# Performance work log

Hardware: AMD Instinct MI355X
Metric: run time of the kernel (lower is better)

The kernel has to match this reference:

```python
import jax, jax.numpy as jnp
import numpy as np

N_ATOMS = 200_000
AVG_NEIGHBORS = 64
N_PAIRS = N_ATOMS * AVG_NEIGHBORS
BOX = 60.0  # Angstrom, so cutoff=10 masks most random pairs (realistic neighbor-list sparsity)


def setup_inputs() -> dict:
    key = jax.random.key(0)
    kR, ki, kj = jax.random.split(key, 3)
    R = jax.random.uniform(kR, (N_ATOMS, 3), dtype=jnp.float32) * BOX
    idx_i = jax.random.randint(ki, (N_PAIRS,), 0, N_ATOMS, dtype=jnp.int32)
    idx_j = jax.random.randint(kj, (N_PAIRS,), 0, N_ATOMS, dtype=jnp.int32)
    # learned scalar parameters from __init__
    epsilon = jnp.float32(0.238)
    sigma = jnp.float32(3.4)
    cutoff = jnp.float32(10.0)
    return {"R": R, "epsilon": epsilon, "sigma": sigma, "cutoff": cutoff,
            "idx_i": idx_i, "idx_j": idx_j}


def reference(R, epsilon, sigma, cutoff, idx_i, idx_j):
    """LJ 12-6 pairwise potential over a neighbor list.

    Returns (energy [N] per-atom, forces [N,3]).
    Each (i,j) pair appears in both directions in the pair list, hence the 0.5
    factor on per-atom energy; forces accumulate per direction (action-reaction
    handled by the symmetric pair list).
    """
    n_atoms = R.shape[0]
    rij = R[idx_i] - R[idx_j]                     # [P,3] gather
    r2 = jnp.sum(rij * rij, axis=-1)              # [P]
    mask = (r2 < cutoff * cutoff) & (r2 > 1e-10)  # inside cutoff, exclude coincident
    r2s = jnp.where(mask, r2, 1.0)                # safe divide
    sr2 = (sigma * sigma) / r2s
    sr6 = sr2 * sr2 * sr2
    sr12 = sr6 * sr6
    e_pair = jnp.where(mask, 4.0 * epsilon * (sr12 - sr6), 0.0)          # [P]
    f_mag = jnp.where(mask, 24.0 * epsilon * (2.0 * sr12 - sr6) / r2s, 0.0)
    f_pair = f_mag[:, None] * rij                 # [P,3]
    energy = 0.5 * jax.ops.segment_sum(e_pair, idx_i, num_segments=n_atoms)   # [N]
    forces = jax.ops.segment_sum(f_pair, idx_i, num_segments=n_atoms)         # [N,3]
    return energy, forces
```

## Files before the change

kernel.cpp:

```cpp
#include <hip/hip_runtime.h>
#include <stdint.h>


typedef int   v4i __attribute__((ext_vector_type(4)));
typedef float v4f __attribute__((ext_vector_type(4)));
typedef float v2f __attribute__((ext_vector_type(2)));

#define GRP    8
#define WGT    1024
#define NWG_F  256

#if __has_builtin(__builtin_amdgcn_global_atomic_fadd_v2f32)
__device__ __forceinline__ void pk_atomic_add(float* p, float a, float b) {
    typedef __attribute__((address_space(1))) v2f gv2f;
    v2f v; v.x = a; v.y = b;
    (void)__builtin_amdgcn_global_atomic_fadd_v2f32((gv2f*)(uintptr_t)p, v);
}
#else
__device__ __forceinline__ void pk_atomic_add(float* p, float a, float b) {
    atomicAdd(p, a);
    atomicAdd(p + 1, b);
}
#endif

__global__ void __launch_bounds__(256) prep_kernel(
    const float* __restrict__ R, const float* __restrict__ cut_p,
    v4f* __restrict__ Rp, unsigned* __restrict__ packed, int n_atoms)
{
    int t = blockIdx.x * blockDim.x + threadIdx.x;
    int n_grp = (n_atoms + 4) / 5;
    if (t >= n_grp) return;
    const float inv_cut = 1.0f / cut_p[0];
    int a0 = t * 5;
    unsigned w = 0u;
#pragma unroll
    for (int k = 0; k < 5; ++k) {
        int a = a0 + k;
        if (a < n_atoms) {
            float x = R[3 * a + 0];
            float y = R[3 * a + 1];
            float z = R[3 * a + 2];
            v4f v; v.x = x; v.y = y; v.z = z; v.w = 0.0f;
            Rp[a] = v;
            int cx = min(7, max(0, (int)(x * inv_cut)));
            int cy = min(7, max(0, (int)(y * inv_cut)));
            w |= (unsigned)(cx | (cy << 3)) << (6 * k);
        }
    }
    packed[t] = w;
}

__global__ void __launch_bounds__(256) pad_R_kernel(
    const float* __restrict__ R, v4f* __restrict__ Rp, int n_atoms)
{
    int a = blockIdx.x * blockDim.x + threadIdx.x;
    if (a < n_atoms) {
        v4f v;
        v.x = R[3 * a + 0];
        v.y = R[3 * a + 1];
        v.z = R[3 * a + 2];
        v.w = 0.0f;
        Rp[a] = v;
    }
}

__device__ __forceinline__ unsigned cell6w(const unsigned* __restrict__ lds32,
                                           unsigned a) {
    unsigned q = __umulhi(a, 0xCCCCCCCDu) >> 2;
    unsigned r = a - q * 5u;
    return (lds32[q] >> (r * 6u)) & 63u;
}

__device__ __forceinline__ void load_grp(
    const int* __restrict__ idx_i, const int* __restrict__ idx_j,
    int p, int n_pairs, int* __restrict__ is8, int* __restrict__ js8)
{
    if (p + GRP <= n_pairs) {
        v4i a0 = __builtin_nontemporal_load((const v4i*)idx_i + (p >> 2));
        v4i a1 = __builtin_nontemporal_load((const v4i*)idx_i + (p >> 2) + 1);
        v4i b0 = __builtin_nontemporal_load((const v4i*)idx_j + (p >> 2));
        v4i b1 = __builtin_nontemporal_load((const v4i*)idx_j + (p >> 2) + 1);
        is8[0] = a0.x; is8[1] = a0.y; is8[2] = a0.z; is8[3] = a0.w;
        is8[4] = a1.x; is8[5] = a1.y; is8[6] = a1.z; is8[7] = a1.w;
        js8[0] = b0.x; js8[1] = b0.y; js8[2] = b0.z; js8[3] = b0.w;
        js8[4] = b1.x; js8[5] = b1.y; js8[6] = b1.z; js8[7] = b1.w;
    } else {
#pragma unroll
        for (int k = 0; k < GRP; ++k) {
            bool v = (p + k < n_pairs);
            is8[k] = v ? idx_i[p + k] : 0;
            js8[k] = v ? idx_j[p + k] : 0;
        }
    }
}

__device__ __forceinline__ void filt_sel(const unsigned* __restrict__ lds32,
                                         int* __restrict__ is8,
                                         int* __restrict__ js8)
{
#pragma unroll
    for (int k = 0; k < GRP; ++k) {
        unsigned ci = cell6w(lds32, (unsigned)is8[k]);
        unsigned cj = cell6w(lds32, (unsigned)js8[k]);
        int ddx = (int)(ci & 7u) - (int)(cj & 7u);
        int ddy = (int)(ci >> 3) - (int)(cj >> 3);
        bool ok = ((unsigned)(ddx + 1) <= 2u) & ((unsigned)(ddy + 1) <= 2u);
        is8[k] = ok ? is8[k] : 0;
        js8[k] = ok ? js8[k] : 0;
    }
}

__device__ __forceinline__ void lj_body_st(
    v4f A, v4f B, float eps, float s2, float cut2, int gi,
    float* __restrict__ st)
{
    const float dx = A.x - B.x, dy = A.y - B.y, dz = A.z - B.z;
    const float r2 = dx * dx + dy * dy + dz * dz;
    if (r2 < cut2 && r2 > 1e-10f) {
        const float inv  = 1.0f / r2;
        const float sr2  = s2 * inv;
        const float sr6  = sr2 * sr2 * sr2;
        const float sr12 = sr6 * sr6;
        const float e    = 2.0f * eps * (sr12 - sr6);
        const float f    = 24.0f * eps * (2.0f * sr12 - sr6) * inv;
        float* p = st + ((size_t)(unsigned)gi << 2);
        pk_atomic_add(p,     e,      f * dx);
        pk_atomic_add(p + 2, f * dy, f * dz);
    }
}

__device__ __forceinline__ void lj_body(
    v4f A, v4f B, float eps, float s2, float cut2, int gi,
    float* __restrict__ energy, float* __restrict__ forces)
{
    const float dx = A.x - B.x, dy = A.y - B.y, dz = A.z - B.z;
    const float r2 = dx * dx + dy * dy + dz * dz;
    if (r2 < cut2 && r2 > 1e-10f) {
        const float inv  = 1.0f / r2;
        const float sr2  = s2 * inv;
        const float sr6  = sr2 * sr2 * sr2;
        const float sr12 = sr6 * sr6;
        const float e    = 2.0f * eps * (sr12 - sr6);
        const float f    = 24.0f * eps * (2.0f * sr12 - sr6) * inv;
        atomicAdd(&energy[gi], e);
        atomicAdd(&forces[3 * gi + 0], f * dx);
        atomicAdd(&forces[3 * gi + 1], f * dy);
        atomicAdd(&forces[3 * gi + 2], f * dz);
    }
}

__global__ void __launch_bounds__(WGT, 4) lj_fused_st_kernel(
    const v4f* __restrict__ Rp,
    const unsigned* __restrict__ packed,
    const int* __restrict__ idx_i,
    const int* __restrict__ idx_j,
    const float* __restrict__ eps_p,
    const float* __restrict__ sig_p,
    const float* __restrict__ cut_p,
    float* __restrict__ st,
    int n_pairs, int pk_words, int chunk)
{
    extern __shared__ unsigned lds[];
    for (int w = threadIdx.x; w < pk_words; w += WGT)
        lds[w] = packed[w];
    __syncthreads();

    const float eps  = eps_p[0];
    const float sig  = sig_p[0];
    const float cut  = cut_p[0];
    const float s2   = sig * sig;
    const float cut2 = cut * cut;

    const int cs = blockIdx.x * chunk;
    const int ce = min(cs + chunk, n_pairs);
    const int STRIDE = WGT * GRP;

    int p0 = cs + (int)threadIdx.x * GRP;
    if (p0 >= ce) return;

    int isA[GRP], jsA[GRP], isB[GRP], jsB[GRP];

    load_grp(idx_i, idx_j, p0, n_pairs, isA, jsA);
    filt_sel(lds, isA, jsA);
    int p1 = p0 + STRIDE;

    while (true) {
        const bool h1 = p1 < ce;

        if (h1) load_grp(idx_i, idx_j, p1, n_pairs, isB, jsB);

        v4f Ri[GRP], Rj[GRP];
#pragma unroll
        for (int k = 0; k < GRP; ++k) { Ri[k] = Rp[isA[k]]; Rj[k] = Rp[jsA[k]]; }

        if (h1) filt_sel(lds, isB, jsB);

#pragma unroll
        for (int k = 0; k < GRP; ++k)
            lj_body_st(Ri[k], Rj[k], eps, s2, cut2, isA[k], st);

        if (!h1) break;
#pragma unroll
        for (int k = 0; k < GRP; ++k) { isA[k] = isB[k]; jsA[k] = jsB[k]; }
        p1 += STRIDE;
    }
}

__global__ void __launch_bounds__(256) finalize_kernel(
    const v4f* __restrict__ st, float* __restrict__ energy,
    float* __restrict__ forces, int n_atoms)
{
    int a = blockIdx.x * blockDim.x + threadIdx.x;
    if (a < n_atoms) {
        v4f s = st[a];
        energy[a]          = s.x;
        forces[3 * a + 0]  = s.y;
        forces[3 * a + 1]  = s.z;
        forces[3 * a + 2]  = s.w;
    }
}

__global__ void __launch_bounds__(WGT, 4) lj_fused_kernel(
    const v4f* __restrict__ Rp,
    const unsigned* __restrict__ packed,
    const int* __restrict__ idx_i,
    const int* __restrict__ idx_j,
    const float* __restrict__ eps_p,
    const float* __restrict__ sig_p,
    const float* __restrict__ cut_p,
    float* __restrict__ energy,
    float* __restrict__ forces,
    int n_pairs, int pk_words, int chunk)
{
    extern __shared__ unsigned lds[];
    for (int w = threadIdx.x; w < pk_words; w += WGT)
        lds[w] = packed[w];
    __syncthreads();

    const float eps  = eps_p[0];
    const float sig  = sig_p[0];
    const float cut  = cut_p[0];
    const float s2   = sig * sig;
    const float cut2 = cut * cut;

    const int cs = blockIdx.x * chunk;
    const int ce = min(cs + chunk, n_pairs);
    const int STRIDE = WGT * GRP;

    int p0 = cs + (int)threadIdx.x * GRP;
    if (p0 >= ce) return;

    int isA[GRP], jsA[GRP], isB[GRP], jsB[GRP];
    load_grp(idx_i, idx_j, p0, n_pairs, isA, jsA);
    filt_sel(lds, isA, jsA);
    int p1 = p0 + STRIDE;

    while (true) {
        const bool h1 = p1 < ce;
        if (h1) load_grp(idx_i, idx_j, p1, n_pairs, isB, jsB);
        v4f Ri[GRP], Rj[GRP];
#pragma unroll
        for (int k = 0; k < GRP; ++k) { Ri[k] = Rp[isA[k]]; Rj[k] = Rp[jsA[k]]; }
        if (h1) filt_sel(lds, isB, jsB);
#pragma unroll
        for (int k = 0; k < GRP; ++k)
            lj_body(Ri[k], Rj[k], eps, s2, cut2, isA[k], energy, forces);
        if (!h1) break;
#pragma unroll
        for (int k = 0; k < GRP; ++k) { isA[k] = isB[k]; jsA[k] = jsB[k]; }
        p1 += STRIDE;
    }
}

#define PPT 8
__global__ void __launch_bounds__(256) lj_pairs_fb_kernel(
    const v4f* __restrict__ Rp,
    const v4i* __restrict__ idx_i4, const v4i* __restrict__ idx_j4,
    const float* __restrict__ eps_p, const float* __restrict__ sig_p,
    const float* __restrict__ cut_p,
    float* __restrict__ energy, float* __restrict__ forces, int n_oct)
{
    int t = blockIdx.x * blockDim.x + threadIdx.x;
    if (t >= n_oct) return;
    const float eps  = eps_p[0];
    const float sig  = sig_p[0];
    const float cut  = cut_p[0];
    const float s2   = sig * sig;
    const float cut2 = cut * cut;
    v4i ii0 = __builtin_nontemporal_load(idx_i4 + 2 * t);
    v4i ii1 = __builtin_nontemporal_load(idx_i4 + 2 * t + 1);
    v4i jj0 = __builtin_nontemporal_load(idx_j4 + 2 * t);
    v4i jj1 = __builtin_nontemporal_load(idx_j4 + 2 * t + 1);
    int is[PPT] = { ii0.x, ii0.y, ii0.z, ii0.w, ii1.x, ii1.y, ii1.z, ii1.w };
    int js[PPT] = { jj0.x, jj0.y, jj0.z, jj0.w, jj1.x, jj1.y, jj1.z, jj1.w };
    v4f Ri[PPT], Rj[PPT];
#pragma unroll
    for (int k = 0; k < PPT; ++k) Ri[k] = Rp[is[k]];
#pragma unroll
    for (int k = 0; k < PPT; ++k) Rj[k] = Rp[js[k]];
#pragma unroll
    for (int k = 0; k < PPT; ++k)
        lj_body(Ri[k], Rj[k], eps, s2, cut2, is[k], energy, forces);
}

__global__ void lj_pairs_fb_tail_kernel(
    const v4f* __restrict__ Rp,
    const int* __restrict__ idx_i, const int* __restrict__ idx_j,
    const float* __restrict__ eps_p, const float* __restrict__ sig_p,
    const float* __restrict__ cut_p,
    float* __restrict__ energy, float* __restrict__ forces,
    int start, int n_pairs)
{
    int p = start + blockIdx.x * blockDim.x + threadIdx.x;
    if (p >= n_pairs) return;
    const float eps = eps_p[0];
    const float sig = sig_p[0];
    const float cut = cut_p[0];
    lj_body(Rp[idx_i[p]], Rp[idx_j[p]], eps, sig * sig, cut * cut,
            idx_i[p], energy, forces);
}

extern "C" void kernel_launch(void* const* d_in, const int* in_sizes, int n_in,
                              void* d_out, int out_size, void* d_ws, size_t ws_size,
                              hipStream_t stream) {
    const float* R     = (const float*)d_in[0];
    const float* eps_p = (const float*)d_in[1];
    const float* sig_p = (const float*)d_in[2];
    const float* cut_p = (const float*)d_in[3];
    const int*   idx_i = (const int*)d_in[4];
    const int*   idx_j = (const int*)d_in[5];

    const int n_atoms = in_sizes[0] / 3;
    const int n_pairs = in_sizes[4];

    float* energy = (float*)d_out;
    float* forces = (float*)d_out + n_atoms;

    char* ws = (char*)d_ws;
    const size_t rp_b     = (((size_t)n_atoms * 16) + 255) & ~(size_t)255;
    const int    pk_words = (n_atoms + 4) / 5;
    const size_t pk_b     = (((size_t)pk_words * 4) + 255) & ~(size_t)255;
    const size_t st_b     = (((size_t)n_atoms * 16) + 255) & ~(size_t)255;
    const size_t lds_b    = (((size_t)pk_words * 4) + 15) & ~(size_t)15;

    const bool have_rp  = ws_size >= rp_b;
    const bool lds_ok   = lds_b <= 160000;
    const bool use_st   = have_rp && lds_ok
                          && (ws_size >= rp_b + pk_b + st_b);
    const bool use_old  = !use_st && have_rp && lds_ok
                          && (ws_size >= rp_b + pk_b);

    v4f*      Rp     = (v4f*)ws;
    unsigned* packed = (unsigned*)(ws + rp_b);
    float*    st     = (float*)(ws + rp_b + pk_b);

    if (use_st) {
        (void)hipMemsetAsync(st, 0, (size_t)n_atoms * 16, stream);

        int pblocks = (pk_words + 255) / 256;
        prep_kernel<<<pblocks, 256, 0, stream>>>(R, cut_p, Rp, packed, n_atoms);

        (void)hipFuncSetAttribute((const void*)lj_fused_st_kernel,
                                  hipFuncAttributeMaxDynamicSharedMemorySize,
                                  (int)lds_b);
        int chunk = (((n_pairs + NWG_F - 1) / NWG_F) + GRP - 1) & ~(GRP - 1);
        lj_fused_st_kernel<<<NWG_F, WGT, lds_b, stream>>>(
            Rp, packed, idx_i, idx_j, eps_p, sig_p, cut_p,
            st, n_pairs, pk_words, chunk);

        int fblocks = (n_atoms + 255) / 256;
        finalize_kernel<<<fblocks, 256, 0, stream>>>(
            (const v4f*)st, energy, forces, n_atoms);
    } else if (use_old) {
        (void)hipMemsetAsync(d_out, 0, (size_t)out_size * sizeof(float), stream);

        int pblocks = (pk_words + 255) / 256;
        prep_kernel<<<pblocks, 256, 0, stream>>>(R, cut_p, Rp, packed, n_atoms);

        (void)hipFuncSetAttribute((const void*)lj_fused_kernel,
                                  hipFuncAttributeMaxDynamicSharedMemorySize,
                                  (int)lds_b);
        int chunk = (((n_pairs + NWG_F - 1) / NWG_F) + GRP - 1) & ~(GRP - 1);
        lj_fused_kernel<<<NWG_F, WGT, lds_b, stream>>>(
            Rp, packed, idx_i, idx_j, eps_p, sig_p, cut_p,
            energy, forces, n_pairs, pk_words, chunk);
    } else if (have_rp) {
        (void)hipMemsetAsync(d_out, 0, (size_t)out_size * sizeof(float), stream);

        int blocks = (n_atoms + 255) / 256;
        pad_R_kernel<<<blocks, 256, 0, stream>>>(R, Rp, n_atoms);
        const int n_oct = n_pairs / PPT;
        const int start = n_oct * PPT;
        if (n_oct > 0) {
            int fblocks = (n_oct + 255) / 256;
            lj_pairs_fb_kernel<<<fblocks, 256, 0, stream>>>(
                Rp, (const v4i*)idx_i, (const v4i*)idx_j,
                eps_p, sig_p, cut_p, energy, forces, n_oct);
        }
        if (start < n_pairs) {
            lj_pairs_fb_tail_kernel<<<1, 64, 0, stream>>>(
                Rp, idx_i, idx_j, eps_p, sig_p, cut_p,
                energy, forces, start, n_pairs);
        }
    }
}
```

Baseline: 191.0 us.

## Compact passing pairs per wave via ballot and LDS before issuing atomics

The 6-bit cell codes are now packed densely, 16 atoms per 3 words, and read as unaligned byte pairs from LDS, which frees LDS space. In that space each wave gets a small staging buffer. Passing LJ pairs are compacted into it with ballot/mbcnt, and the lanes then issue atomics from the packed buffer, so atomics run on contiguous active lanes instead of sparse divergent ones. In exchange, the packed v2f atomics are replaced by four scalar atomics, LDS traffic and wave-uniform loop control are added, and pairs that overflow the buffer fall back to direct atomics.

```diff
diff --git a/kernel.cpp b/kernel.cpp
--- a/kernel.cpp
+++ b/kernel.cpp
@@ -4,38 +4,27 @@
 
 typedef int   v4i __attribute__((ext_vector_type(4)));
 typedef float v4f __attribute__((ext_vector_type(4)));
-typedef float v2f __attribute__((ext_vector_type(2)));
 
 #define GRP    8
 #define WGT    1024
 #define NWG_F  256
-
-#if __has_builtin(__builtin_amdgcn_global_atomic_fadd_v2f32)
-__device__ __forceinline__ void pk_atomic_add(float* p, float a, float b) {
-    typedef __attribute__((address_space(1))) v2f gv2f;
-    v2f v; v.x = a; v.y = b;
-    (void)__builtin_amdgcn_global_atomic_fadd_v2f32((gv2f*)(uintptr_t)p, v);
-}
-#else
-__device__ __forceinline__ void pk_atomic_add(float* p, float a, float b) {
-    atomicAdd(p, a);
-    atomicAdd(p + 1, b);
-}
-#endif
+#define SLOTS  31
 
 __global__ void __launch_bounds__(256) prep_kernel(
     const float* __restrict__ R, const float* __restrict__ cut_p,
     v4f* __restrict__ Rp, unsigned* __restrict__ packed, int n_atoms)
 {
     int t = blockIdx.x * blockDim.x + threadIdx.x;
-    int n_grp = (n_atoms + 4) / 5;
-    if (t >= n_grp) return;
+    int n_thr = (n_atoms + 15) >> 4;
+    if (t == 0) packed[3 * n_thr] = 0u;
+    if (t >= n_thr) return;
     const float inv_cut = 1.0f / cut_p[0];
-    int a0 = t * 5;
-    unsigned w = 0u;
-#pragma unroll
-    for (int k = 0; k < 5; ++k) {
+    int a0 = t << 4;
+    unsigned w[3] = {0u, 0u, 0u};
+#pragma unroll
+    for (int k = 0; k < 16; ++k) {
         int a = a0 + k;
+        unsigned c = 0u;
         if (a < n_atoms) {
             float x = R[3 * a + 0];
             float y = R[3 * a + 1];
@@ -44,10 +33,15 @@
             Rp[a] = v;
             int cx = min(7, max(0, (int)(x * inv_cut)));
             int cy = min(7, max(0, (int)(y * inv_cut)));
-            w |= (unsigned)(cx | (cy << 3)) << (6 * k);
-        }
-    }
-    packed[t] = w;
+            c = (unsigned)(cx | (cy << 3));
+        }
+        int bit = 6 * k, word = bit >> 5, off = bit & 31;
+        w[word] |= c << off;
+        if (off > 26) w[word + 1] |= c >> (32 - off);
+    }
+    packed[3 * t + 0] = w[0];
+    packed[3 * t + 1] = w[1];
+    packed[3 * t + 2] = w[2];
 }
 
 __global__ void __launch_bounds__(256) pad_R_kernel(
@@ -64,11 +58,11 @@
     }
 }
 
-__device__ __forceinline__ unsigned cell6w(const unsigned* __restrict__ lds32,
-                                           unsigned a) {
-    unsigned q = __umulhi(a, 0xCCCCCCCDu) >> 2;
-    unsigned r = a - q * 5u;
-    return (lds32[q] >> (r * 6u)) & 63u;
+__device__ __forceinline__ unsigned cell6(const unsigned char* c8, unsigned a) {
+    unsigned bit = a * 6u;
+    unsigned by  = bit >> 3;
+    unsigned v   = (unsigned)c8[by] | ((unsigned)c8[by + 1] << 8);
+    return (v >> (bit & 7u)) & 63u;
 }
 
 __device__ __forceinline__ void load_grp(
@@ -94,38 +88,31 @@
     }
 }
 
-__device__ __forceinline__ void filt_sel(const unsigned* __restrict__ lds32,
+__device__ __forceinline__ void load_or_zero(
+    const int* __restrict__ idx_i, const int* __restrict__ idx_j,
+    int p, int ce, int n_pairs, int* __restrict__ is8, int* __restrict__ js8)
+{
+    if (p < ce) {
+        load_grp(idx_i, idx_j, p, n_pairs, is8, js8);
+    } else {
+#pragma unroll
+        for (int k = 0; k < GRP; ++k) { is8[k] = 0; js8[k] = 0; }
+    }
+}
+
+__device__ __forceinline__ void filt_sel(const unsigned char* __restrict__ c8,
                                          int* __restrict__ is8,
                                          int* __restrict__ js8)
 {
 #pragma unroll
     for (int k = 0; k < GRP; ++k) {
-        unsigned ci = cell6w(lds32, (unsigned)is8[k]);
-        unsigned cj = cell6w(lds32, (unsigned)js8[k]);
+        unsigned ci = cell6(c8, (unsigned)is8[k]);
+        unsigned cj = cell6(c8, (unsigned)js8[k]);
         int ddx = (int)(ci & 7u) - (int)(cj & 7u);
         int ddy = (int)(ci >> 3) - (int)(cj >> 3);
         bool ok = ((unsigned)(ddx + 1) <= 2u) & ((unsigned)(ddy + 1) <= 2u);
         is8[k] = ok ? is8[k] : 0;
         js8[k] = ok ? js8[k] : 0;
-    }
-}
-
-__device__ __forceinline__ void lj_body_st(
-    v4f A, v4f B, float eps, float s2, float cut2, int gi,
-    float* __restrict__ st)
-{
-    const float dx = A.x - B.x, dy = A.y - B.y, dz = A.z - B.z;
-    const float r2 = dx * dx + dy * dy + dz * dz;
-    if (r2 < cut2 && r2 > 1e-10f) {
-        const float inv  = 1.0f / r2;
-        const float sr2  = s2 * inv;
-        const float sr6  = sr2 * sr2 * sr2;
-        const float sr12 = sr6 * sr6;
-        const float e    = 2.0f * eps * (sr12 - sr6);
-        const float f    = 24.0f * eps * (2.0f * sr12 - sr6) * inv;
-        float* p = st + ((size_t)(unsigned)gi << 2);
-        pk_atomic_add(p,     e,      f * dx);
-        pk_atomic_add(p + 2, f * dy, f * dz);
     }
 }
 
@@ -158,12 +145,15 @@
     const float* __restrict__ sig_p,
     const float* __restrict__ cut_p,
     float* __restrict__ st,
-    int n_pairs, int pk_words, int chunk)
+    int n_pairs, int pk_words, int chunk, int buf_off)
 {
     extern __shared__ unsigned lds[];
     for (int w = threadIdx.x; w < pk_words; w += WGT)
         lds[w] = packed[w];
     __syncthreads();
+    const unsigned char* c8 = (const unsigned char*)lds;
+    unsigned* mybuf = lds + buf_off + (threadIdx.x >> 6) * (SLOTS * 5);
+    const int lane = (int)(threadIdx.x & 63u);
 
     const float eps  = eps_p[0];
     const float sig  = sig_p[0];
@@ -173,36 +163,83 @@
 
     const int cs = blockIdx.x * chunk;
     const int ce = min(cs + chunk, n_pairs);
-    const int STRIDE = WGT * GRP;
-
-    int p0 = cs + (int)threadIdx.x * GRP;
-    if (p0 >= ce) return;
+    const int S  = WGT * GRP;
+    const int n_iter = (ce > cs) ? (ce - cs + S - 1) / S : 0;
+    if (n_iter == 0) return;
 
     int isA[GRP], jsA[GRP], isB[GRP], jsB[GRP];
-
-    load_grp(idx_i, idx_j, p0, n_pairs, isA, jsA);
-    filt_sel(lds, isA, jsA);
-    int p1 = p0 + STRIDE;
-
-    while (true) {
-        const bool h1 = p1 < ce;
-
-        if (h1) load_grp(idx_i, idx_j, p1, n_pairs, isB, jsB);
+    int pA = cs + (int)threadIdx.x * GRP;
+
+    load_or_zero(idx_i, idx_j, pA, ce, n_pairs, isA, jsA);
+    filt_sel(c8, isA, jsA);
+
+    for (int it = 0; it < n_iter; ++it) {
+        const bool hB = (it + 1 < n_iter);
+        const int  pB = pA + S;
+
+        if (hB) load_or_zero(idx_i, idx_j, pB, ce, n_pairs, isB, jsB);
 
         v4f Ri[GRP], Rj[GRP];
 #pragma unroll
         for (int k = 0; k < GRP; ++k) { Ri[k] = Rp[isA[k]]; Rj[k] = Rp[jsA[k]]; }
 
-        if (h1) filt_sel(lds, isB, jsB);
-
-#pragma unroll
-        for (int k = 0; k < GRP; ++k)
-            lj_body_st(Ri[k], Rj[k], eps, s2, cut2, isA[k], st);
-
-        if (!h1) break;
-#pragma unroll
-        for (int k = 0; k < GRP; ++k) { isA[k] = isB[k]; jsA[k] = jsB[k]; }
-        p1 += STRIDE;
+        if (hB) filt_sel(c8, isB, jsB);
+
+        unsigned base = 0u;
+#pragma unroll
+        for (int k = 0; k < GRP; ++k) {
+            const v4f A = Ri[k], B = Rj[k];
+            const float dx = A.x - B.x, dy = A.y - B.y, dz = A.z - B.z;
+            const float r2 = dx * dx + dy * dy + dz * dz;
+            const bool pass = (r2 < cut2) & (r2 > 1e-10f);
+            const float inv  = 1.0f / r2;
+            const float sr2  = s2 * inv;
+            const float sr6  = sr2 * sr2 * sr2;
+            const float sr12 = sr6 * sr6;
+            const float e    = 2.0f * eps * (sr12 - sr6);
+            const float f    = 24.0f * eps * (2.0f * sr12 - sr6) * inv;
+
+            unsigned long long bal = __ballot(pass);
+            if (pass) {
+                int before = __builtin_amdgcn_mbcnt_hi(
+                    (unsigned)(bal >> 32),
+                    __builtin_amdgcn_mbcnt_lo((unsigned)bal, 0u));
+                int slot = (int)base + before;
+                if (slot < SLOTS) {
+                    unsigned* b = mybuf + slot * 5;
+                    b[0] = (unsigned)isA[k];
+                    b[1] = __float_as_uint(e);
+                    b[2] = __float_as_uint(f * dx);
+                    b[3] = __float_as_uint(f * dy);
+                    b[4] = __float_as_uint(f * dz);
+                } else {
+                    float* p = st + ((size_t)(unsigned)isA[k] << 2);
+                    atomicAdd(p + 0, e);
+                    atomicAdd(p + 1, f * dx);
+                    atomicAdd(p + 2, f * dy);
+                    atomicAdd(p + 3, f * dz);
+                }
+            }
+            base += (unsigned)__popcll(bal);
+            if (base > SLOTS) base = SLOTS;
+        }
+
+        const int nb = (int)base;
+        if (nb > 0 && lane < nb) {
+            unsigned* b = mybuf + lane * 5;
+            unsigned gi = b[0];
+            float* p = st + ((size_t)gi << 2);
+            atomicAdd(p + 0, __uint_as_float(b[1]));
+            atomicAdd(p + 1, __uint_as_float(b[2]));
+            atomicAdd(p + 2, __uint_as_float(b[3]));
+            atomicAdd(p + 3, __uint_as_float(b[4]));
+        }
+
+        if (hB) {
+#pragma unroll
+            for (int k = 0; k < GRP; ++k) { isA[k] = isB[k]; jsA[k] = jsB[k]; }
+            pA = pB;
+        }
     }
 }
 
@@ -236,6 +273,7 @@
     for (int w = threadIdx.x; w < pk_words; w += WGT)
         lds[w] = packed[w];
     __syncthreads();
+    const unsigned char* c8 = (const unsigned char*)lds;
 
     const float eps  = eps_p[0];
     const float sig  = sig_p[0];
@@ -245,15 +283,15 @@
 
     const int cs = blockIdx.x * chunk;
     const int ce = min(cs + chunk, n_pairs);
-    const int STRIDE = WGT * GRP;
+    const int S  = WGT * GRP;
 
     int p0 = cs + (int)threadIdx.x * GRP;
     if (p0 >= ce) return;
 
     int isA[GRP], jsA[GRP], isB[GRP], jsB[GRP];
     load_grp(idx_i, idx_j, p0, n_pairs, isA, jsA);
-    filt_sel(lds, isA, jsA);
-    int p1 = p0 + STRIDE;
+    filt_sel(c8, isA, jsA);
+    int p1 = p0 + S;
 
     while (true) {
         const bool h1 = p1 < ce;
@@ -261,14 +299,14 @@
         v4f Ri[GRP], Rj[GRP];
 #pragma unroll
         for (int k = 0; k < GRP; ++k) { Ri[k] = Rp[isA[k]]; Rj[k] = Rp[jsA[k]]; }
-        if (h1) filt_sel(lds, isB, jsB);
+        if (h1) filt_sel(c8, isB, jsB);
 #pragma unroll
         for (int k = 0; k < GRP; ++k)
             lj_body(Ri[k], Rj[k], eps, s2, cut2, isA[k], energy, forces);
         if (!h1) break;
 #pragma unroll
         for (int k = 0; k < GRP; ++k) { isA[k] = isB[k]; jsA[k] = jsB[k]; }
-        p1 += STRIDE;
+        p1 += S;
     }
 }
 
@@ -338,16 +376,20 @@
 
     char* ws = (char*)d_ws;
     const size_t rp_b     = (((size_t)n_atoms * 16) + 255) & ~(size_t)255;
-    const int    pk_words = (n_atoms + 4) / 5;
+    const int    n_thr16  = (n_atoms + 15) >> 4;
+    const int    pk_words = 3 * n_thr16 + 1;
     const size_t pk_b     = (((size_t)pk_words * 4) + 255) & ~(size_t)255;
     const size_t st_b     = (((size_t)n_atoms * 16) + 255) & ~(size_t)255;
-    const size_t lds_b    = (((size_t)pk_words * 4) + 15) & ~(size_t)15;
+
+    const int    buf_off  = (pk_words + 3) & ~3;
+    const size_t lds_b    = ((size_t)buf_off + 16u * SLOTS * 5u) * 4u;
+    const size_t ldsF_b   = (((size_t)pk_words * 4) + 15) & ~(size_t)15;
 
     const bool have_rp  = ws_size >= rp_b;
     const bool lds_ok   = lds_b <= 160000;
     const bool use_st   = have_rp && lds_ok
                           && (ws_size >= rp_b + pk_b + st_b);
-    const bool use_old  = !use_st && have_rp && lds_ok
+    const bool use_old  = !use_st && have_rp && (ldsF_b <= 160000)
                           && (ws_size >= rp_b + pk_b);
 
     v4f*      Rp     = (v4f*)ws;
@@ -357,7 +399,7 @@
     if (use_st) {
         (void)hipMemsetAsync(st, 0, (size_t)n_atoms * 16, stream);
 
-        int pblocks = (pk_words + 255) / 256;
+        int pblocks = (n_thr16 + 255) / 256;
         prep_kernel<<<pblocks, 256, 0, stream>>>(R, cut_p, Rp, packed, n_atoms);
 
         (void)hipFuncSetAttribute((const void*)lj_fused_st_kernel,
@@ -366,7 +408,7 @@
         int chunk = (((n_pairs + NWG_F - 1) / NWG_F) + GRP - 1) & ~(GRP - 1);
         lj_fused_st_kernel<<<NWG_F, WGT, lds_b, stream>>>(
             Rp, packed, idx_i, idx_j, eps_p, sig_p, cut_p,
-            st, n_pairs, pk_words, chunk);
+            st, n_pairs, pk_words, chunk, buf_off);
 
         int fblocks = (n_atoms + 255) / 256;
         finalize_kernel<<<fblocks, 256, 0, stream>>>(
@@ -374,14 +416,14 @@
     } else if (use_old) {
         (void)hipMemsetAsync(d_out, 0, (size_t)out_size * sizeof(float), stream);
 
-        int pblocks = (pk_words + 255) / 256;
+        int pblocks = (n_thr16 + 255) / 256;
         prep_kernel<<<pblocks, 256, 0, stream>>>(R, cut_p, Rp, packed, n_atoms);
 
         (void)hipFuncSetAttribute((const void*)lj_fused_kernel,
                                   hipFuncAttributeMaxDynamicSharedMemorySize,
-                                  (int)lds_b);
+                                  (int)ldsF_b);
         int chunk = (((n_pairs + NWG_F - 1) / NWG_F) + GRP - 1) & ~(GRP - 1);
-        lj_fused_kernel<<<NWG_F, WGT, lds_b, stream>>>(
+        lj_fused_kernel<<<NWG_F, WGT, ldsF_b, stream>>>(
             Rp, packed, idx_i, idx_j, eps_p, sig_p, cut_p,
             energy, forces, n_pairs, pk_words, chunk);
     } else if (have_rp) {
```

New measurement: 194.3 us. No clear change (+1.7%).
